# Kernel optimization log

Hardware: AMD Instinct MI355X
Metric: run time of the kernel (lower is better)

## Reference

```python
import jax, jax.numpy as jnp
import numpy as np

N, C, T, V = 16, 64, 634, 26
K, TK = 3, 9          # spatial / temporal kernel sizes
NCLS, NAE = 60, 4     # num_classes, num_att_edge
D = C * V             # transformer d_model = 1664
NH = 4
HD = D // NH
DFF = 128
EPS = 1e-5


def _bn(x, g, b, m, v, axis=1):
    # inference-mode BatchNorm with running stats
    sh = [1] * x.ndim
    sh[axis] = -1
    return (x - m.reshape(sh)) * jax.lax.rsqrt(v.reshape(sh) + EPS) * g.reshape(sh) + b.reshape(sh)


def _ln(x, g, b):
    mu = x.mean(-1, keepdims=True)
    var = jnp.mean((x - mu) ** 2, -1, keepdims=True)
    return (x - mu) * jax.lax.rsqrt(var + EPS) * g + b


def setup_inputs() -> dict:
    ks = iter(jax.random.split(jax.random.key(0), 64))
    nrm = lambda sh, s=0.05: jax.random.normal(next(ks), sh, jnp.float32) * s
    pos = lambda sh: jax.random.uniform(next(ks), sh, jnp.float32) * 0.5 + 0.5
    return dict(
        x=jax.random.normal(next(ks), (N, C, T, V), jnp.float32),
        A=jax.random.uniform(next(ks), (K, V, V), jnp.float32) / V,
        sgc_w=nrm((3, K * C, C)), sgc_b=nrm((3, K * C)),
        M=jnp.ones((3, K, V, V), jnp.float32),
        bnA_g=pos((3, C)), bnA_b=nrm((3, C)), bnA_m=nrm((3, C)), bnA_v=pos((3, C)),
        tconv_w=nrm((3, C, C, TK)), tconv_b=nrm((3, C)),
        bnB_g=pos((3, C)), bnB_b=nrm((3, C)), bnB_m=nrm((3, C)), bnB_v=pos((3, C)),
        fc_w=nrm((NCLS, C)), fc_b=nrm((NCLS,)),
        attbn_g=pos((C,)), attbn_b=nrm((C,)), attbn_m=nrm((C,)), attbn_v=pos((C,)),
        tbn_g=pos((T,)), tbn_b=nrm((T,)), tbn_m=nrm((T,)), tbn_v=pos((T,)),
        attn_w=nrm((4, D, D), 0.02), attn_b=nrm((4, D)),
        ln1_g=pos((D,)), ln1_b=nrm((D,)),
        ff1_w=nrm((D, DFF), 0.02), ff1_b=nrm((DFF,)),
        ff2_w=nrm((DFF, D), 0.02), ff2_b=nrm((D,)),
        ln2_g=pos((D,)), ln2_b=nrm((D,)),
        attconv_w=nrm((NCLS, C)),
        nodeconv_w=nrm((1, NCLS)),
        nodebn_g=pos((1,)), nodebn_b=nrm((1,)), nodebn_m=nrm((1,)), nodebn_v=pos((1,)),
        edgeconv_w=nrm((NAE * V, NCLS)),
        edgebn_g=pos((NAE * V,)), edgebn_b=nrm((NAE * V,)), edgebn_m=nrm((NAE * V,)), edgebn_v=pos((NAE * V,)),
    )


def reference(x, A, sgc_w, sgc_b, M, bnA_g, bnA_b, bnA_m, bnA_v, tconv_w, tconv_b,
              bnB_g, bnB_b, bnB_m, bnB_v, fc_w, fc_b, attbn_g, attbn_b, attbn_m, attbn_v,
              tbn_g, tbn_b, tbn_m, tbn_v, attn_w, attn_b, ln1_g, ln1_b, ff1_w, ff1_b,
              ff2_w, ff2_b, ln2_g, ln2_b, attconv_w, nodeconv_w, nodebn_g, nodebn_b,
              nodebn_m, nodebn_v, edgeconv_w, edgebn_g, edgebn_b, edgebn_m, edgebn_v):
    h = x
    for i in range(3):  # three STGC blocks (eval-mode BN, dropout off)
        y = jnp.einsum('nctv,oc->notv', h, sgc_w[i]) + sgc_b[i][None, :, None, None]
        y = y.reshape(N, K, C, T, V)
        y = jnp.einsum('nkctv,kvw->nctw', y, A * M[i])          # spatial graph conv
        y = jax.nn.relu(_bn(y, bnA_g[i], bnA_b[i], bnA_m[i], bnA_v[i]))
        y = jax.lax.conv_general_dilated(
            y, tconv_w[i][:, :, :, None], (1, 1),
            ((TK // 2, TK // 2), (0, 0)),
            dimension_numbers=('NCHW', 'OIHW', 'NCHW')) + tconv_b[i][None, :, None, None]
        h = jax.nn.relu(_bn(y, bnB_g[i], bnB_b[i], bnB_m[i], bnB_v[i]))
    # classification head: global avg pool + 1x1 conv (== linear)
    output = h.mean((2, 3)) @ fc_w.T + fc_b                     # [N, NCLS]
    x_att = _bn(h, attbn_g, attbn_b, attbn_m, attbn_v)
    # transformer branch: computed in the original but its result is never
    # used by the returned tensors (att_mat is only printed)
    xt = h.transpose(0, 2, 1, 3).reshape(N, T, D)
    xt = _bn(xt, tbn_g, tbn_b, tbn_m, tbn_v, axis=1)            # BatchNorm1d over T channels
    q, k, v = (((xt @ attn_w[j] + attn_b[j]).reshape(N, T, NH, HD).transpose(0, 2, 1, 3)) for j in range(3))
    attn = jax.nn.softmax(jnp.einsum('nhqd,nhkd->nhqk', q, k) / HD ** 0.5, axis=-1)
    ao = jnp.einsum('nhqk,nhkd->nhqd', attn, v).transpose(0, 2, 1, 3).reshape(N, T, D)
    ao = ao @ attn_w[3] + attn_b[3]
    xb = _ln(xt + ao, ln1_g, ln1_b)
    ff = jax.nn.relu(xb @ ff1_w + ff1_b) @ ff2_w + ff2_b
    _dead = _ln(xb + ff, ln2_g, ln2_b)                          # dead: not returned
    # node attention
    x_att = jnp.einsum('nctv,oc->notv', x_att, attconv_w)       # [N, NCLS, T, V]
    x_node = jnp.einsum('nctv,oc->notv', x_att, nodeconv_w)     # [N, 1, T, V]
    x_node = _bn(x_node, nodebn_g, nodebn_b, nodebn_m, nodebn_v)
    att_node = jax.nn.sigmoid(x_node)                           # interpolate to (T,V) is identity here
    # edge attention
    x_edge = x_att.mean(2, keepdims=True)                       # avg pool over T: [N, NCLS, 1, V]
    x_edge = jnp.einsum('nctv,oc->notv', x_edge, edgeconv_w)    # [N, NAE*V, 1, V]
    x_edge = _bn(x_edge, edgebn_g, edgebn_b, edgebn_m, edgebn_v)
    att_edge = jax.nn.relu(jnp.tanh(x_edge.reshape(N, NAE, V, V)))
    return (output, att_node, att_edge)
```

## Files before the change

### kernel.cpp

```cpp
#include <hip/hip_runtime.h>
#include <hip/hip_bf16.h>
#include <math.h>

#define NN 16
#define CC 64
#define TT_ 634
#define VV 26
#define TV 16484
#define KK 3
#define OO 192
#define TKK 9
#define NCLS 60
#define NAE 4
#define EPS 1e-5f

typedef __attribute__((ext_vector_type(8))) short short8;
typedef __attribute__((ext_vector_type(4))) float f32x4;

static __device__ __forceinline__ float bf2f(unsigned int u) {
  union { unsigned int i; float f; } v; v.i = u << 16; return v.f;
}
static __device__ __forceinline__ unsigned int f2bf(float x) {
  union { float f; unsigned int i; } v; v.f = x;
  unsigned int r = v.i + 0x7fffu + ((v.i >> 16) & 1u);
  return r >> 16;
}

#define W1_ELEMS (3 * OO * CC)
#define W2_ELEMS (3 * CC * 576)
#define AM_ELEMS (3 * KK * 1024)

__global__ __launch_bounds__(256) void k_prep_all(
    const float* __restrict__ sgc_w, const float* __restrict__ tconv_w,
    const float* __restrict__ Ap, const float* __restrict__ Mp,
    unsigned short* __restrict__ W1all, unsigned short* __restrict__ W2all,
    unsigned short* __restrict__ AMall)
{
  int j = blockIdx.x * 256 + threadIdx.x;
  if (j < W1_ELEMS) { W1all[j] = (unsigned short)f2bf(sgc_w[j]); return; }
  j -= W1_ELEMS;
  if (j < W2_ELEMS) {
    const int i = j / (CC * 576), r = j % (CC * 576);
    const int c = r / 576, q = r % 576, dt = q >> 6, ci = q & 63;
    W2all[j] = (unsigned short)f2bf(
        tconv_w[(size_t)i * CC * CC * TKK + c * 576 + ci * 9 + dt]);
    return;
  }
  j -= W2_ELEMS;
  if (j < AM_ELEMS) {
    const int i = j / (KK * 1024), r = j % (KK * 1024);
    const int k = r >> 10, rr = r & 1023;
    const int w = rr >> 5, v = rr & 31;
    float val = 0.f;
    if (w < VV && v < VV)
      val = Ap[(k * VV + v) * VV + w] *
            Mp[((size_t)i * KK + k) * VV * VV + v * VV + w];
    AMall[j] = (unsigned short)f2bf(val);
  }
}

template<int F32IN>
__global__ __launch_bounds__(256) void k_fused_sgc(
    const void* __restrict__ hin,
    const unsigned short* __restrict__ W1,
    const float* __restrict__ Wb,
    const unsigned short* __restrict__ AMk,
    const float* __restrict__ bg, const float* __restrict__ bb,
    const float* __restrict__ bm, const float* __restrict__ bv,
    unsigned short* __restrict__ hout)
{
  const int NTT = 159;
  const int n = blockIdx.x / NTT, tt = blockIdx.x % NTT;
  const int t0 = tt << 2;
  const int f0 = t0 * VV;
  const int tid = threadIdx.x;
  const int wv = tid >> 6, lane = tid & 63;
  const int l15 = lane & 15, l4 = lane >> 4;

  __shared__ unsigned short sH[112 * 64];
  __shared__ unsigned short sY[192 * 120];
  __shared__ float sWb[OO];
  __shared__ float sS[CC], sOff[CC];

  short8 amf[KK][2];
  #pragma unroll
  for (int k = 0; k < KK; ++k)
    #pragma unroll
    for (int nf = 0; nf < 2; ++nf)
      amf[k][nf] = *(const short8*)(AMk + (k << 10) + ((nf * 16 + l15) << 5)
                                    + (l4 << 3));

  const int wm0 = wv * 48;
  short8 afr[2][3];
  #pragma unroll
  for (int ks = 0; ks < 2; ++ks)
    #pragma unroll
    for (int mf = 0; mf < 3; ++mf)
      afr[ks][mf] = *(const short8*)(W1 + (size_t)(wm0 + mf * 16 + l15) * CC
                                     + (ks << 5) + (l4 << 3));

  if (tid < OO) {
    sWb[tid] = Wb[tid];
  } else if (tid >= 192) {
    const int c = tid - 192;
    const float s = bg[c] * rsqrtf(bv[c] + EPS);
    sS[c] = s;
    sOff[c] = bb[c] - bm[c] * s;
  }

  for (int it = tid; it < 14 * 64; it += 256) {
    const int ci = it & 63, fc = it >> 6;
    const int flb = fc << 3;
    const int fg = f0 + flb;
    unsigned short e[8];
    if (flb >= 104) {
      #pragma unroll
      for (int j = 0; j < 8; ++j) e[j] = 0;
    } else if (F32IN) {
      const float* hb = (const float*)hin + ((size_t)n * CC + ci) * TV;
      if (fg + 8 <= TV) {
        const float4 v0 = *(const float4*)(hb + fg);
        const float4 v1 = *(const float4*)(hb + fg + 4);
        e[0] = (unsigned short)f2bf(v0.x); e[1] = (unsigned short)f2bf(v0.y);
        e[2] = (unsigned short)f2bf(v0.z); e[3] = (unsigned short)f2bf(v0.w);
        e[4] = (unsigned short)f2bf(v1.x); e[5] = (unsigned short)f2bf(v1.y);
        e[6] = (unsigned short)f2bf(v1.z); e[7] = (unsigned short)f2bf(v1.w);
      } else {
        #pragma unroll
        for (int j = 0; j < 8; ++j)
          e[j] = (fg + j < TV) ? (unsigned short)f2bf(hb[fg + j])
                               : (unsigned short)0;
      }
    } else {
      const unsigned short* hb = (const unsigned short*)hin
                                 + ((size_t)n * CC + ci) * TV;
      if (fg + 8 <= TV) {
        const uint2 v0 = *(const uint2*)(hb + fg);
        const uint2 v1 = *(const uint2*)(hb + fg + 4);
        e[0] = (unsigned short)(v0.x & 0xffffu); e[1] = (unsigned short)(v0.x >> 16);
        e[2] = (unsigned short)(v0.y & 0xffffu); e[3] = (unsigned short)(v0.y >> 16);
        e[4] = (unsigned short)(v1.x & 0xffffu); e[5] = (unsigned short)(v1.x >> 16);
        e[6] = (unsigned short)(v1.y & 0xffffu); e[7] = (unsigned short)(v1.y >> 16);
      } else {
        #pragma unroll
        for (int j = 0; j < 8; ++j)
          e[j] = (fg + j < TV) ? hb[fg + j] : (unsigned short)0;
      }
    }
    const int cg8 = ci >> 3, cl = ci & 7;
    #pragma unroll
    for (int j = 0; j < 8; ++j)
      sH[((flb + j) << 6) + ((cg8 ^ j) << 3) + cl] = e[j];
  }
  __syncthreads();

  f32x4 acc[3][7] = {};
  #pragma unroll
  for (int ks = 0; ks < 2; ++ks) {
    short8 bfr[7];
    const int cg = (ks << 2) + l4;
    #pragma unroll
    for (int nf = 0; nf < 7; ++nf) {
      const int fl = nf * 16 + l15;
      bfr[nf] = *(const short8*)&sH[(fl << 6) + ((cg ^ (fl & 7)) << 3)];
    }
    #pragma unroll
    for (int mf = 0; mf < 3; ++mf)
      #pragma unroll
      for (int nf = 0; nf < 7; ++nf)
        acc[mf][nf] = __builtin_amdgcn_mfma_f32_16x16x32_bf16(
            afr[ks][mf], bfr[nf], acc[mf][nf], 0, 0, 0);
  }
  #pragma unroll
  for (int mf = 0; mf < 3; ++mf)
    #pragma unroll
    for (int r = 0; r < 4; ++r) {
      const int o = wm0 + mf * 16 + (l4 << 2) + r;
      const float bias = sWb[o];
      unsigned short* yr = &sY[o * 120 + l15];
      #pragma unroll
      for (int nf = 0; nf < 7; ++nf)
        yr[nf * 16] = (unsigned short)f2bf(acc[mf][nf][r] + bias);
    }
  __syncthreads();

  const int t = t0 + wv;
  if (t < TT_) {
    f32x4 a2[4][2] = {};
    const int cuoff = wv * 13 + (l4 << 2);
    #pragma unroll
    for (int k = 0; k < KK; ++k)
      #pragma unroll
      for (int mf = 0; mf < 4; ++mf) {
        const unsigned int* rb =
            (const unsigned int*)&sY[(k * 64 + mf * 16 + l15) * 120];
        union { unsigned int u[4]; short8 s; } av;
        av.u[0] = rb[cuoff];     av.u[1] = rb[cuoff + 1];
        av.u[2] = rb[cuoff + 2]; av.u[3] = rb[cuoff + 3];
        #pragma unroll
        for (int nf = 0; nf < 2; ++nf)
          a2[mf][nf] = __builtin_amdgcn_mfma_f32_16x16x32_bf16(
              av.s, amf[k][nf], a2[mf][nf], 0, 0, 0);
      }
    #pragma unroll
    for (int mf = 0; mf < 4; ++mf)
      #pragma unroll
      for (int r = 0; r < 4; ++r) {
        const int c = mf * 16 + (l4 << 2) + r;
        const float s = sS[c], off = sOff[c];
        unsigned short* op = hout + ((size_t)n * CC + c) * TV + t * VV;
        op[l15] = (unsigned short)f2bf(fmaxf(fmaf(a2[mf][0][r], s, off), 0.f));
        if (l15 < 10)
          op[16 + l15] =
              (unsigned short)f2bf(fmaxf(fmaf(a2[mf][1][r], s, off), 0.f));
      }
  }
}

template<int F32OUT>
__global__ __launch_bounds__(256) void k_tconv_mfma(
    const unsigned short* __restrict__ xin,
    const unsigned short* __restrict__ W2,
    const float* __restrict__ wb, const float* __restrict__ bg,
    const float* __restrict__ bb, const float* __restrict__ bm,
    const float* __restrict__ bv, void* __restrict__ xout)
{
  const int NFT = (TV + 255) >> 8;
  const int n = blockIdx.x / NFT, ft = blockIdx.x % NFT;
  const int f0 = ft << 8;
  const int tid = threadIdx.x;
  const int w = tid >> 6, lane = tid & 63;
  const int l15 = lane & 15, l4 = lane >> 4;
  __shared__ unsigned short sIn[464 * 64];

  const unsigned short* xb = xin + (size_t)n * CC * TV;
  for (int it = tid; it < 58 * 64; it += 256) {
    const int ci = it & 63, fc = it >> 6;
    const int flb = fc << 3;
    const int fg = f0 - 104 + flb;
    unsigned short e[8];
    if (fg >= 0 && fg + 8 <= TV) {
      const uint2 v0 = *(const uint2*)(xb + (size_t)ci * TV + fg);
      const uint2 v1 = *(const uint2*)(xb + (size_t)ci * TV + fg + 4);
      e[0] = (unsigned short)(v0.x & 0xffffu); e[1] = (unsigned short)(v0.x >> 16);
      e[2] = (unsigned short)(v0.y & 0xffffu); e[3] = (unsigned short)(v0.y >> 16);
      e[4] = (unsigned short)(v1.x & 0xffffu); e[5] = (unsigned short)(v1.x >> 16);
      e[6] = (unsigned short)(v1.y & 0xffffu); e[7] = (unsigned short)(v1.y >> 16);
    } else {
      #pragma unroll
      for (int j = 0; j < 8; ++j) {
        const int f = fg + j;
        e[j] = (f >= 0 && f < TV) ? xb[(size_t)ci * TV + f] : (unsigned short)0;
      }
    }
    const int cg8 = ci >> 3, cl = ci & 7;
    #pragma unroll
    for (int j = 0; j < 8; ++j) {
      sIn[((flb + j) << 6) + ((cg8 ^ j) << 3) + cl] = e[j];
    }
  }
  __syncthreads();

  const int w64 = w << 6;
  f32x4 acc[4][4] = {};
  short8 aCur[4], aNxt[4];
  {
    const int koff = (l4 << 3);
    #pragma unroll
    for (int mt = 0; mt < 4; ++mt)
      aCur[mt] = *(const short8*)(W2 + (size_t)(mt * 16 + l15) * 576 + koff);
  }
  for (int s = 0; s < 18; ++s) {
    if (s < 17) {
      const int s1 = s + 1;
      const int koff = ((s1 >> 1) << 6) + ((s1 & 1) << 5) + (l4 << 3);
      #pragma unroll
      for (int mt = 0; mt < 4; ++mt)
        aNxt[mt] = *(const short8*)(W2 + (size_t)(mt * 16 + l15) * 576 + koff);
    }
    const int dt = s >> 1;
    const int cg = ((s & 1) << 2) + l4;
    const int flb = w64 + l15 + (dt - 4) * 26 + 104;
    short8 bfrag[4];
    #pragma unroll
    for (int nt = 0; nt < 4; ++nt) {
      const int fl = flb + (nt << 4);
      bfrag[nt] = *(const short8*)&sIn[(fl << 6) + ((cg ^ (fl & 7)) << 3)];
    }
    #pragma unroll
    for (int mt = 0; mt < 4; ++mt)
      #pragma unroll
      for (int nt = 0; nt < 4; ++nt)
        acc[mt][nt] = __builtin_amdgcn_mfma_f32_16x16x32_bf16(
            aCur[mt], bfrag[nt], acc[mt][nt], 0, 0, 0);
    if (s < 17) {
      #pragma unroll
      for (int mt = 0; mt < 4; ++mt) aCur[mt] = aNxt[mt];
    }
  }

  #pragma unroll
  for (int mt = 0; mt < 4; ++mt) {
    #pragma unroll
    for (int r = 0; r < 4; ++r) {
      const int c = mt * 16 + (l4 << 2) + r;
      const float sc = bg[c] * rsqrtf(bv[c] + EPS);
      const float off = fmaf(wb[c] - bm[c], sc, bb[c]);
      #pragma unroll
      for (int nt = 0; nt < 4; ++nt) {
        const int f = f0 + w64 + (nt << 4) + l15;
        if (f < TV) {
          const float val = fmaxf(fmaf(acc[mt][nt][r], sc, off), 0.f);
          if (F32OUT)
            ((float*)xout)[((size_t)n * CC + c) * TV + f] = val;
          else
            ((unsigned short*)xout)[((size_t)n * CC + c) * TV + f] =
                (unsigned short)f2bf(val);
        }
      }
    }
  }
}

__global__ __launch_bounds__(256) void k_pool(
    const float* __restrict__ h, float* __restrict__ pooled,
    float* __restrict__ hmeanv)
{
  const int tid = threadIdx.x;
  const int bid = blockIdx.x;
  const float* row = h + (size_t)bid * TV;
  __shared__ float part[9 * VV];
  if (tid < 9 * VV) {
    const int tt = tid / VV, v = tid - tt * VV;
    float s = 0.f;
    for (int t = tt; t < TT_; t += 9) s += row[t * VV + v];
    part[tid] = s;
  }
  __syncthreads();
  if (tid < VV) {
    float tot = 0.f;
    #pragma unroll
    for (int j = 0; j < 9; ++j) tot += part[j * VV + tid];
    hmeanv[(size_t)bid * VV + tid] = tot / (float)TT_;
    part[tid] = tot;
  }
  __syncthreads();
  if (tid == 0) {
    float tot = 0.f;
    for (int v = 0; v < VV; ++v) tot += part[v];
    pooled[bid] = tot / (float)TV;
  }
}

__global__ __launch_bounds__(256) void k_head_edge(
    const float* __restrict__ pooled, const float* __restrict__ hmeanv,
    const float* __restrict__ fcw, const float* __restrict__ fcb,
    const float* __restrict__ ag, const float* __restrict__ ab,
    const float* __restrict__ am, const float* __restrict__ av,
    const float* __restrict__ attw, const float* __restrict__ edgew,
    const float* __restrict__ eg, const float* __restrict__ eb,
    const float* __restrict__ em, const float* __restrict__ ev,
    float* __restrict__ dout)
{
  const int tid = threadIdx.x;
  const int n = blockIdx.x;
  __shared__ float sbnm[CC * VV];
  __shared__ float sxam[NCLS * VV];
  __shared__ float spool[CC];
  for (int i = tid; i < CC * VV; i += 256) {
    const int c = i / VV;
    const float s = ag[c] * rsqrtf(av[c] + EPS);
    const float off = ab[c] - am[c] * s;
    sbnm[i] = fmaf(hmeanv[(size_t)(n * CC) * VV + i], s, off);
  }
  if (tid < CC) spool[tid] = pooled[n * CC + tid];
  __syncthreads();
  for (int i = tid; i < NCLS * VV; i += 256) {
    const int o = i / VV, v = i - o * VV;
    float a = 0.f;
    for (int c = 0; c < CC; ++c) a = fmaf(attw[o * CC + c], sbnm[c * VV + v], a);
    sxam[i] = a;
  }
  if (tid < NCLS) {
    float a = fcb[tid];
    for (int c = 0; c < CC; ++c) a = fmaf(spool[c], fcw[tid * CC + c], a);
    dout[n * NCLS + tid] = a;
  }
  __syncthreads();
  for (int i = tid; i < NAE * VV * VV; i += 256) {
    const int j = i / VV, v = i - j * VV;
    float a = 0.f;
    for (int o = 0; o < NCLS; ++o) a = fmaf(edgew[j * NCLS + o], sxam[o * VV + v], a);
    const float s = eg[j] * rsqrtf(ev[j] + EPS);
    const float val = tanhf(fmaf(a - em[j], s, eb[j]));
    dout[NN * NCLS + (size_t)NN * TV + (size_t)n * NAE * VV * VV + i] = fmaxf(val, 0.f);
  }
}

__global__ __launch_bounds__(256) void k_node(
    const float* __restrict__ h,
    const float* __restrict__ ag, const float* __restrict__ ab,
    const float* __restrict__ am, const float* __restrict__ av,
    const float* __restrict__ attw, const float* __restrict__ nodew,
    const float* __restrict__ ng, const float* __restrict__ nb,
    const float* __restrict__ nm, const float* __restrict__ nv,
    float* __restrict__ dout)
{
  const int tid = threadIdx.x;
  __shared__ float ac[CC];
  __shared__ float tmp[CC];
  if (tid < CC) {
    float nc = 0.f;
    for (int o = 0; o < NCLS; ++o) nc = fmaf(nodew[o], attw[o * CC + tid], nc);
    const float s = ag[tid] * rsqrtf(av[tid] + EPS);
    const float off = ab[tid] - am[tid] * s;
    ac[tid] = nc * s;
    tmp[tid] = nc * off;
  }
  __syncthreads();
  if (tid == 0) {
    float b = 0.f;
    for (int c = 0; c < CC; ++c) b += tmp[c];
    tmp[0] = b;
  }
  __syncthreads();
  const float b0 = tmp[0];
  const size_t i = (size_t)blockIdx.x * 256 + tid;
  if (i < (size_t)NN * TV) {
    const int n = (int)(i / TV), f = (int)(i - (size_t)n * TV);
    const float* hb = h + (size_t)n * CC * TV + f;
    float xsum = b0;
    #pragma unroll 8
    for (int c = 0; c < CC; ++c) xsum = fmaf(hb[(size_t)c * TV], ac[c], xsum);
    const float s = ng[0] * rsqrtf(nv[0] + EPS);
    const float y = fmaf(xsum - nm[0], s, nb[0]);
    dout[NN * NCLS + i] = 1.f / (1.f + expf(-y));
  }
}

extern "C" void kernel_launch(void* const* d_in, const int* in_sizes, int n_in,
                              void* d_out, int out_size, void* d_ws, size_t ws_size,
                              hipStream_t stream) {
  const float* x        = (const float*)d_in[0];
  const float* A        = (const float*)d_in[1];
  const float* sgc_w    = (const float*)d_in[2];
  const float* sgc_b    = (const float*)d_in[3];
  const float* M        = (const float*)d_in[4];
  const float* bnA_g    = (const float*)d_in[5];
  const float* bnA_b    = (const float*)d_in[6];
  const float* bnA_m    = (const float*)d_in[7];
  const float* bnA_v    = (const float*)d_in[8];
  const float* tconv_w  = (const float*)d_in[9];
  const float* tconv_b  = (const float*)d_in[10];
  const float* bnB_g    = (const float*)d_in[11];
  const float* bnB_b    = (const float*)d_in[12];
  const float* bnB_m    = (const float*)d_in[13];
  const float* bnB_v    = (const float*)d_in[14];
  const float* fc_w     = (const float*)d_in[15];
  const float* fc_b     = (const float*)d_in[16];
  const float* attbn_g  = (const float*)d_in[17];
  const float* attbn_b  = (const float*)d_in[18];
  const float* attbn_m  = (const float*)d_in[19];
  const float* attbn_v  = (const float*)d_in[20];
  const float* attconv_w  = (const float*)d_in[35];
  const float* nodeconv_w = (const float*)d_in[36];
  const float* nodebn_g   = (const float*)d_in[37];
  const float* nodebn_b   = (const float*)d_in[38];
  const float* nodebn_m   = (const float*)d_in[39];
  const float* nodebn_v   = (const float*)d_in[40];
  const float* edgeconv_w = (const float*)d_in[41];
  const float* edgebn_g   = (const float*)d_in[42];
  const float* edgebn_b   = (const float*)d_in[43];
  const float* edgebn_m   = (const float*)d_in[44];
  const float* edgebn_v   = (const float*)d_in[45];

  float* pooled = (float*)d_ws;
  float* hmeanv = pooled + NN * CC;
  unsigned short* W1all = (unsigned short*)(hmeanv + (size_t)NN * CC * VV);
  unsigned short* W2all = W1all + W1_ELEMS;
  unsigned short* AMall = W2all + W2_ELEMS;
  unsigned short* bufA  = AMall + AM_ELEMS;
  unsigned short* bufBh = bufA + (size_t)NN * CC * TV;
  float* bufB = (float*)(bufBh + (size_t)NN * CC * TV);
  float* out = (float*)d_out;

  const int PREP_TOT = W1_ELEMS + W2_ELEMS + AM_ELEMS;
  k_prep_all<<<(PREP_TOT + 255) / 256, 256, 0, stream>>>(
      sgc_w, tconv_w, A, M, W1all, W2all, AMall);

  const int GF = NN * 159;
  const int NFC = (TV + 255) >> 8;
  for (int i = 0; i < 3; ++i) {
    const unsigned short* W1i = W1all + (size_t)i * OO * CC;
    const unsigned short* W2i = W2all + (size_t)i * CC * 576;
    const unsigned short* AMi = AMall + (size_t)i * KK * 1024;
    if (i == 0)
      k_fused_sgc<1><<<GF, 256, 0, stream>>>(
          x, W1i, sgc_b, AMi,
          bnA_g, bnA_b, bnA_m, bnA_v, bufA);
    else
      k_fused_sgc<0><<<GF, 256, 0, stream>>>(
          bufBh, W1i, sgc_b + i * OO, AMi,
          bnA_g + i * CC, bnA_b + i * CC, bnA_m + i * CC, bnA_v + i * CC,
          bufA);
    if (i < 2)
      k_tconv_mfma<0><<<NN * NFC, 256, 0, stream>>>(
          bufA, W2i, tconv_b + i * CC,
          bnB_g + i * CC, bnB_b + i * CC, bnB_m + i * CC, bnB_v + i * CC,
          (void*)bufBh);
    else
      k_tconv_mfma<1><<<NN * NFC, 256, 0, stream>>>(
          bufA, W2i, tconv_b + i * CC,
          bnB_g + i * CC, bnB_b + i * CC, bnB_m + i * CC, bnB_v + i * CC,
          (void*)bufB);
  }
  k_pool<<<NN * CC, 256, 0, stream>>>(bufB, pooled, hmeanv);
  k_head_edge<<<NN, 256, 0, stream>>>(pooled, hmeanv, fc_w, fc_b,
      attbn_g, attbn_b, attbn_m, attbn_v, attconv_w, edgeconv_w,
      edgebn_g, edgebn_b, edgebn_m, edgebn_v, out);
  k_node<<<((size_t)NN * TV + 255) / 256, 256, 0, stream>>>(
      bufB, attbn_g, attbn_b, attbn_m, attbn_v, attconv_w, nodeconv_w,
      nodebn_g, nodebn_b, nodebn_m, nodebn_v, out);
}
```

Before: 633.0 us.

## Cut LDS in sgc and tconv kernels, swap MFMA operands for vector stores

The fused SGC kernel now aliases its input staging buffer onto the output staging buffer, with an extra barrier between the GEMM and the writeback, so it uses less LDS. The temporal-conv kernel stages input channels in two 32-channel halves to halve its LDS footprint, changing the swizzle to match. It also swaps the MFMA A/B operands so each lane holds four consecutive time-vertex outputs, which allows float4/uint2 vectorized global stores. The intent is higher occupancy and fewer store instructions, at the cost of an extra barrier and a serialized reload per channel half.

```diff
diff --git a/kernel.cpp b/kernel.cpp
--- a/kernel.cpp
+++ b/kernel.cpp
@@ -77,10 +77,10 @@
   const int wv = tid >> 6, lane = tid & 63;
   const int l15 = lane & 15, l4 = lane >> 4;
 
-  __shared__ unsigned short sH[112 * 64];
   __shared__ unsigned short sY[192 * 120];
   __shared__ float sWb[OO];
   __shared__ float sS[CC], sOff[CC];
+  unsigned short* sH = sY;
 
   short8 amf[KK][2];
   #pragma unroll
@@ -171,6 +171,8 @@
         acc[mf][nf] = __builtin_amdgcn_mfma_f32_16x16x32_bf16(
             afr[ks][mf], bfr[nf], acc[mf][nf], 0, 0, 0);
   }
+  __syncthreads();
+
   #pragma unroll
   for (int mf = 0; mf < 3; ++mf)
     #pragma unroll
@@ -231,91 +233,99 @@
   const int tid = threadIdx.x;
   const int w = tid >> 6, lane = tid & 63;
   const int l15 = lane & 15, l4 = lane >> 4;
-  __shared__ unsigned short sIn[464 * 64];
+  __shared__ unsigned short sIn[464 * 32];
 
   const unsigned short* xb = xin + (size_t)n * CC * TV;
-  for (int it = tid; it < 58 * 64; it += 256) {
-    const int ci = it & 63, fc = it >> 6;
-    const int flb = fc << 3;
-    const int fg = f0 - 104 + flb;
-    unsigned short e[8];
-    if (fg >= 0 && fg + 8 <= TV) {
-      const uint2 v0 = *(const uint2*)(xb + (size_t)ci * TV + fg);
-      const uint2 v1 = *(const uint2*)(xb + (size_t)ci * TV + fg + 4);
-      e[0] = (unsigned short)(v0.x & 0xffffu); e[1] = (unsigned short)(v0.x >> 16);
-      e[2] = (unsigned short)(v0.y & 0xffffu); e[3] = (unsigned short)(v0.y >> 16);
-      e[4] = (unsigned short)(v1.x & 0xffffu); e[5] = (unsigned short)(v1.x >> 16);
-      e[6] = (unsigned short)(v1.y & 0xffffu); e[7] = (unsigned short)(v1.y >> 16);
-    } else {
-      #pragma unroll
-      for (int j = 0; j < 8; ++j) {
-        const int f = fg + j;
-        e[j] = (f >= 0 && f < TV) ? xb[(size_t)ci * TV + f] : (unsigned short)0;
-      }
-    }
-    const int cg8 = ci >> 3, cl = ci & 7;
-    #pragma unroll
-    for (int j = 0; j < 8; ++j) {
-      sIn[((flb + j) << 6) + ((cg8 ^ j) << 3) + cl] = e[j];
-    }
-  }
-  __syncthreads();
-
   const int w64 = w << 6;
   f32x4 acc[4][4] = {};
-  short8 aCur[4], aNxt[4];
-  {
-    const int koff = (l4 << 3);
-    #pragma unroll
-    for (int mt = 0; mt < 4; ++mt)
-      aCur[mt] = *(const short8*)(W2 + (size_t)(mt * 16 + l15) * 576 + koff);
-  }
-  for (int s = 0; s < 18; ++s) {
-    if (s < 17) {
-      const int s1 = s + 1;
-      const int koff = ((s1 >> 1) << 6) + ((s1 & 1) << 5) + (l4 << 3);
+
+  for (int cc = 0; cc < 2; ++cc) {
+    if (cc) __syncthreads();
+    for (int it = tid; it < 58 * 32; it += 256) {
+      const int ci = it & 31, fc = it >> 5;
+      const int flb = fc << 3;
+      const int fg = f0 - 104 + flb;
+      const int cig = (cc << 5) + ci;
+      unsigned short e[8];
+      if (fg >= 0 && fg + 8 <= TV) {
+        const uint2 v0 = *(const uint2*)(xb + (size_t)cig * TV + fg);
+        const uint2 v1 = *(const uint2*)(xb + (size_t)cig * TV + fg + 4);
+        e[0] = (unsigned short)(v0.x & 0xffffu); e[1] = (unsigned short)(v0.x >> 16);
+        e[2] = (unsigned short)(v0.y & 0xffffu); e[3] = (unsigned short)(v0.y >> 16);
+        e[4] = (unsigned short)(v1.x & 0xffffu); e[5] = (unsigned short)(v1.x >> 16);
+        e[6] = (unsigned short)(v1.y & 0xffffu); e[7] = (unsigned short)(v1.y >> 16);
+      } else {
+        #pragma unroll
+        for (int j = 0; j < 8; ++j) {
+          const int f = fg + j;
+          e[j] = (f >= 0 && f < TV) ? xb[(size_t)cig * TV + f] : (unsigned short)0;
+        }
+      }
+      const int cg8 = ci >> 3, cl = ci & 7;
+      #pragma unroll
+      for (int j = 0; j < 8; ++j) {
+        const int fl = flb + j;
+        sIn[(fl << 5) + ((cg8 ^ ((fl >> 1) & 3)) << 3) + cl] = e[j];
+      }
+    }
+    __syncthreads();
+
+    short8 wCur[4], wNxt[4];
+    {
+      const int koff = (cc << 5) + (l4 << 3);
       #pragma unroll
       for (int mt = 0; mt < 4; ++mt)
-        aNxt[mt] = *(const short8*)(W2 + (size_t)(mt * 16 + l15) * 576 + koff);
-    }
-    const int dt = s >> 1;
-    const int cg = ((s & 1) << 2) + l4;
-    const int flb = w64 + l15 + (dt - 4) * 26 + 104;
-    short8 bfrag[4];
-    #pragma unroll
-    for (int nt = 0; nt < 4; ++nt) {
-      const int fl = flb + (nt << 4);
-      bfrag[nt] = *(const short8*)&sIn[(fl << 6) + ((cg ^ (fl & 7)) << 3)];
-    }
-    #pragma unroll
-    for (int mt = 0; mt < 4; ++mt)
-      #pragma unroll
-      for (int nt = 0; nt < 4; ++nt)
-        acc[mt][nt] = __builtin_amdgcn_mfma_f32_16x16x32_bf16(
-            aCur[mt], bfrag[nt], acc[mt][nt], 0, 0, 0);
-    if (s < 17) {
-      #pragma unroll
-      for (int mt = 0; mt < 4; ++mt) aCur[mt] = aNxt[mt];
+        wCur[mt] = *(const short8*)(W2 + (size_t)(mt * 16 + l15) * 576 + koff);
+    }
+    for (int dt = 0; dt < TKK; ++dt) {
+      if (dt < 8) {
+        const int koff = ((dt + 1) << 6) + (cc << 5) + (l4 << 3);
+        #pragma unroll
+        for (int mt = 0; mt < 4; ++mt)
+          wNxt[mt] = *(const short8*)(W2 + (size_t)(mt * 16 + l15) * 576 + koff);
+      }
+      const int flb = w64 + l15 + (dt - 4) * 26 + 104;
+      short8 ifr[4];
+      #pragma unroll
+      for (int nt = 0; nt < 4; ++nt) {
+        const int fl = flb + (nt << 4);
+        ifr[nt] = *(const short8*)&sIn[(fl << 5)
+                                       + ((l4 ^ ((fl >> 1) & 3)) << 3)];
+      }
+      #pragma unroll
+      for (int mt = 0; mt < 4; ++mt)
+        #pragma unroll
+        for (int nt = 0; nt < 4; ++nt)
+          acc[mt][nt] = __builtin_amdgcn_mfma_f32_16x16x32_bf16(
+              ifr[nt], wCur[mt], acc[mt][nt], 0, 0, 0);
+      if (dt < 8) {
+        #pragma unroll
+        for (int mt = 0; mt < 4; ++mt) wCur[mt] = wNxt[mt];
+      }
     }
   }
 
   #pragma unroll
   for (int mt = 0; mt < 4; ++mt) {
-    #pragma unroll
-    for (int r = 0; r < 4; ++r) {
-      const int c = mt * 16 + (l4 << 2) + r;
-      const float sc = bg[c] * rsqrtf(bv[c] + EPS);
-      const float off = fmaf(wb[c] - bm[c], sc, bb[c]);
-      #pragma unroll
-      for (int nt = 0; nt < 4; ++nt) {
-        const int f = f0 + w64 + (nt << 4) + l15;
-        if (f < TV) {
-          const float val = fmaxf(fmaf(acc[mt][nt][r], sc, off), 0.f);
-          if (F32OUT)
-            ((float*)xout)[((size_t)n * CC + c) * TV + f] = val;
-          else
-            ((unsigned short*)xout)[((size_t)n * CC + c) * TV + f] =
-                (unsigned short)f2bf(val);
+    const int c = mt * 16 + l15;
+    const float sc = bg[c] * rsqrtf(bv[c] + EPS);
+    const float off = fmaf(wb[c] - bm[c], sc, bb[c]);
+    #pragma unroll
+    for (int nt = 0; nt < 4; ++nt) {
+      const int fbase = f0 + w64 + (nt << 4) + (l4 << 2);
+      if (fbase < TV) {
+        float v0 = fmaxf(fmaf(acc[mt][nt][0], sc, off), 0.f);
+        float v1 = fmaxf(fmaf(acc[mt][nt][1], sc, off), 0.f);
+        float v2 = fmaxf(fmaf(acc[mt][nt][2], sc, off), 0.f);
+        float v3 = fmaxf(fmaf(acc[mt][nt][3], sc, off), 0.f);
+        if (F32OUT) {
+          float4 o4; o4.x = v0; o4.y = v1; o4.z = v2; o4.w = v3;
+          *(float4*)((float*)xout + ((size_t)n * CC + c) * TV + fbase) = o4;
+        } else {
+          uint2 pk;
+          pk.x = f2bf(v0) | (f2bf(v1) << 16);
+          pk.y = f2bf(v2) | (f2bf(v3) << 16);
+          *(uint2*)((unsigned short*)xout + ((size_t)n * CC + c) * TV + fbase) = pk;
         }
       }
     }
```

After: 597.7 us. 1.06x faster.
